# Optimization experiments

Measured on AMD Instinct MI355X. Metric: run time of the kernel, lower is better.

Reference implementation:

```python
import jax, jax.numpy as jnp
import numpy as np

N = 50000      # nodes
E = 800000     # edges (before self loops)
H = 2          # attention heads
CH = 64        # per-head hidden channels
IN = 128       # input features
OUT = 64       # output channels
EPS = 1e-5     # batchnorm eps
SLOPE = 0.2    # LeakyReLU negative slope


def _gat_conv(x, src, dst, W, a_src, a_dst, b, concat):
    # x: [N, Fin]; W: [Fin, H*C]; a_src/a_dst: [H, C]
    n = x.shape[0]
    h = (x @ W).reshape(n, H, -1)                       # [N, H, C]
    al_s = (h * a_src).sum(-1)                          # [N, H]
    al_d = (h * a_dst).sum(-1)                          # [N, H]
    e = al_s[src] + al_d[dst]                           # [E, H]
    e = jnp.where(e > 0, e, SLOPE * e)                  # LeakyReLU
    # softmax over edges grouped by destination node
    m = jax.ops.segment_max(e, dst, num_segments=n)
    ex = jnp.exp(e - m[dst])
    den = jax.ops.segment_sum(ex, dst, num_segments=n)
    alpha = ex / (den[dst] + 1e-16)                     # [E, H]
    out = jax.ops.segment_sum(h[src] * alpha[:, :, None], dst, num_segments=n)
    out = out.reshape(n, -1) if concat else out.mean(axis=1)
    return out + b


def _batchnorm(x, g, be):
    mu = x.mean(axis=0)
    var = x.var(axis=0)  # biased, as torch BN uses in training
    return (x - mu) * jax.lax.rsqrt(var + EPS) * g + be


def setup_inputs() -> dict:
    key = jax.random.key(0)
    ks = jax.random.split(key, 18)
    s = 0.1
    inp = {
        "x": jax.random.normal(ks[0], (N, IN), jnp.float32),
        "edge_index": jax.random.randint(ks[1], (2, E), 0, N, jnp.int64),
        # layer 0: IN -> H*CH (concat)
        "W0": jax.random.normal(ks[2], (IN, H * CH), jnp.float32) * s,
        "a_src0": jax.random.normal(ks[3], (H, CH), jnp.float32) * s,
        "a_dst0": jax.random.normal(ks[4], (H, CH), jnp.float32) * s,
        "b0": jnp.zeros((H * CH,), jnp.float32),
        "g0": jnp.ones((H * CH,), jnp.float32),
        "be0": jnp.zeros((H * CH,), jnp.float32),
        # layer 1: H*CH -> H*CH (concat)
        "W1": jax.random.normal(ks[5], (H * CH, H * CH), jnp.float32) * s,
        "a_src1": jax.random.normal(ks[6], (H, CH), jnp.float32) * s,
        "a_dst1": jax.random.normal(ks[7], (H, CH), jnp.float32) * s,
        "b1": jnp.zeros((H * CH,), jnp.float32),
        "g1": jnp.ones((H * CH,), jnp.float32),
        "be1": jnp.zeros((H * CH,), jnp.float32),
        # layer 2: H*CH -> OUT, concat=False (mean over heads)
        "W2": jax.random.normal(ks[8], (H * CH, H * OUT), jnp.float32) * s,
        "a_src2": jax.random.normal(ks[9], (H, OUT), jnp.float32) * s,
        "a_dst2": jax.random.normal(ks[10], (H, OUT), jnp.float32) * s,
        "b2": jnp.zeros((OUT,), jnp.float32),
    }
    return inp


def reference(x, edge_index, W0, a_src0, a_dst0, b0, g0, be0,
              W1, a_src1, a_dst1, b1, g1, be1,
              W2, a_src2, a_dst2, b2):
    # add self loops (PyG GATConv default)
    loop = jnp.arange(N, dtype=edge_index.dtype)
    src = jnp.concatenate([edge_index[0], loop])
    dst = jnp.concatenate([edge_index[1], loop])

    h = _gat_conv(x, src, dst, W0, a_src0, a_dst0, b0, concat=True)
    h = jax.nn.relu(_batchnorm(h, g0, be0))
    # dropout: eval mode (identity)
    h = _gat_conv(h, src, dst, W1, a_src1, a_dst1, b1, concat=True)
    h = jax.nn.relu(_batchnorm(h, g1, be1))
    out = _gat_conv(h, src, dst, W2, a_src2, a_dst2, b2, concat=False)
    return out
```

## Files before the change

kernel.cpp:

```cpp
#include <hip/hip_runtime.h>


#define N_NODES 50000
#define N_EDGES 800000
#define ET (N_EDGES + N_NODES)
#define FDIM 128
#define SLOPE 0.2f
#define BN_EPS 1e-5f
#define SCAN_NB 196
#define HIST_NB 3321
#define RPK_NB 216
#define LOG2E 1.44269504088896340736f
#define WSTRIDE 18432

typedef __attribute__((ext_vector_type(8))) short bf16x8;
typedef __attribute__((ext_vector_type(4))) float f32x4;
typedef __attribute__((ext_vector_type(8))) unsigned short u16x8;

__device__ __forceinline__ unsigned short f2bf(float f) {
  unsigned u = __float_as_uint(f);
  u = u + 0x7fffu + ((u >> 16) & 1u);
  return (unsigned short)(u >> 16);
}
__device__ __forceinline__ unsigned packbf(float lo, float hi) {
  return ((unsigned)f2bf(hi) << 16) | (unsigned)f2bf(lo);
}
__device__ __forceinline__ float bflo(unsigned p) { return __uint_as_float(p << 16); }
__device__ __forceinline__ float bfhi(unsigned p) { return __uint_as_float(p & 0xffff0000u); }

__global__ __launch_bounds__(256) void build_pre(const int* __restrict__ dst,
                                                 int* __restrict__ counts,
                                                 int* __restrict__ rank,
                                                 const float* __restrict__ W0,
                                                 const float* __restrict__ W1,
                                                 const float* __restrict__ W2,
                                                 const float* __restrict__ as0,
                                                 const float* __restrict__ as1,
                                                 const float* __restrict__ as2,
                                                 const float* __restrict__ ad0,
                                                 const float* __restrict__ ad1,
                                                 const float* __restrict__ ad2,
                                                 unsigned short* __restrict__ Wr) {
  int bid = blockIdx.x;
  if (bid < HIST_NB) {
    int i = bid * 256 + threadIdx.x;
    if (i >= ET) return;
    int d = (i < N_EDGES) ? dst[i] : i - N_EDGES;
    rank[i] = atomicAdd(&counts[d], 1);
    return;
  }
  int i = (bid - HIST_NB) * 256 + threadIdx.x;
  if (i >= 3 * WSTRIDE) return;
  int L = i / WSTRIDE, rem = i % WSTRIDE;
  int t  = rem >> 11;
  int ks = (rem >> 9) & 3;
  int ln = (rem >> 3) & 63;
  int j  = rem & 7;
  int k  = ks * 32 + (ln >> 4) * 8 + j;
  const float* W = (L == 0) ? W0 : ((L == 1) ? W1 : W2);
  float val;
  if (t < 8) {
    int col = t * 16 + (ln & 15);
    val = W[k * 128 + col];
  } else {
    int cl = ln & 15;
    if (cl < 4) {
      int head = cl & 1;
      const float* a = (cl < 2) ? ((L == 0) ? as0 : (L == 1) ? as1 : as2)
                                : ((L == 0) ? ad0 : (L == 1) ? ad1 : ad2);
      float s = 0.f;
      const float* wrow = W + k * 128 + head * 64;
      const float* ah = a + head * 64;
#pragma unroll 8
      for (int c = 0; c < 64; ++c) s = fmaf(wrow[c], ah[c], s);
      val = s * LOG2E;
    } else {
      val = 0.f;
    }
  }
  Wr[i] = f2bf(val);
}


__global__ __launch_bounds__(256) void scan_blk(const int* __restrict__ counts,
                                                int* __restrict__ rowptr,
                                                int* __restrict__ partials) {
  int i = blockIdx.x * 256 + threadIdx.x;
  int lane = threadIdx.x & 63, wv = threadIdx.x >> 6;
  int c = (i < N_NODES) ? counts[i] : 0;
  int v = c;
#pragma unroll
  for (int off = 1; off < 64; off <<= 1) {
    int u = __shfl_up(v, off);
    if (lane >= off) v += u;
  }
  __shared__ int wsum[4];
  if (lane == 63) wsum[wv] = v;
  __syncthreads();
  int add = 0;
  for (int w = 0; w < wv; ++w) add += wsum[w];
  if (i < N_NODES) rowptr[i] = v - c + add;
  if (threadIdx.x == 255) partials[blockIdx.x] = add + v;
}

__global__ __launch_bounds__(256) void scan_fin(int* __restrict__ rowptr,
                                                const int* __restrict__ partials) {
  __shared__ int sh[256];
  int t = threadIdx.x;
  sh[t] = (t < (int)blockIdx.x && t < SCAN_NB) ? partials[t] : 0;
  __syncthreads();
#pragma unroll
  for (int off = 128; off > 0; off >>= 1) {
    if (t < off) sh[t] += sh[t + off];
    __syncthreads();
  }
  int base = sh[0];
  int i = blockIdx.x * 256 + t;
  if (i < N_NODES) rowptr[i] += base;
  if (i == 0) rowptr[N_NODES] = ET;
}

__global__ __launch_bounds__(256) void scatter_pos(const int* __restrict__ src,
                                                   const int* __restrict__ dst,
                                                   const int* __restrict__ rowptr,
                                                   const int* __restrict__ rank,
                                                   int* __restrict__ csr_src) {
  int i = blockIdx.x * 256 + threadIdx.x;
  if (i >= ET) return;
  int d, s;
  if (i < N_EDGES) { d = dst[i]; s = src[i]; } else { d = s = i - N_EDGES; }
  csr_src[rowptr[d] + rank[i]] = s;
}

__global__ __launch_bounds__(128) void bn_fin(float* __restrict__ part,
                                              const float* __restrict__ g,
                                              const float* __restrict__ be,
                                              float* __restrict__ lsbuf) {
  int t = threadIdx.x;
  float s = 0.f, q = 0.f;
#pragma unroll
  for (int k = 0; k < 32; ++k) {
    s += part[k * 256 + t];
    q += part[k * 256 + 128 + t];
    part[k * 256 + t] = 0.f;
    part[k * 256 + 128 + t] = 0.f;
  }
  float mu  = s * (1.f / N_NODES);
  float var = q * (1.f / N_NODES) - mu * mu;
  float sc  = rsqrtf(var + BN_EPS) * g[t];
  lsbuf[t]       = sc;
  lsbuf[128 + t] = be[t] - mu * sc;
}

__global__ __launch_bounds__(256) void gemm_mfma(const void* __restrict__ Xin,
                                                 const unsigned short* __restrict__ WrL,
                                                 const float* __restrict__ lsbuf,
                                                 unsigned short* __restrict__ Hbf,
                                                 float* __restrict__ als,
                                                 float* __restrict__ ald,
                                                 int inBF) {
  __shared__ unsigned short lds[4][16][128];
  __shared__ float ls_scale[128], ls_shift[128];
  int lane = threadIdx.x & 63;
  int wv   = threadIdx.x >> 6;

  if (inBF) {
    int t = threadIdx.x;
    if (t < 128) {
      ls_scale[t] = lsbuf[t];
      ls_shift[t] = lsbuf[128 + t];
    }
    __syncthreads();
  }

  int row0 = blockIdx.x * 64 + wv * 16;
  int gidx = lane & 15;
  int quad = lane >> 4;
  int rA   = row0 + gidx;
  int rAc  = rA < N_NODES ? rA : N_NODES - 1;
  int koff = quad * 8;

  f32x4 acc[9] = {};
#pragma unroll
  for (int ks = 0; ks < 4; ++ks) {
    int cb = ks * 32 + koff;
    float xv[8];
    if (inBF) {
      const uint4* xr = (const uint4*)((const unsigned*)Xin + (size_t)rAc * 64 + (cb >> 1));
      uint4 xa = *xr;
      xv[0] = bflo(xa.x); xv[1] = bfhi(xa.x);
      xv[2] = bflo(xa.y); xv[3] = bfhi(xa.y);
      xv[4] = bflo(xa.z); xv[5] = bfhi(xa.z);
      xv[6] = bflo(xa.w); xv[7] = bfhi(xa.w);
    } else {
      const float4* xr = (const float4*)((const float*)Xin + (size_t)rAc * FDIM + cb);
      float4 xa = xr[0], xb = xr[1];
      xv[0] = xa.x; xv[1] = xa.y; xv[2] = xa.z; xv[3] = xa.w;
      xv[4] = xb.x; xv[5] = xb.y; xv[6] = xb.z; xv[7] = xb.w;
    }
    bf16x8 afrag;
    if (inBF) {
#pragma unroll
      for (int j = 0; j < 8; ++j) {
        int c = cb + j;
        float v = fmaf(xv[j], ls_scale[c], ls_shift[c]);
        v = v > 0.f ? v : 0.f;
        afrag[j] = (short)f2bf(v);
      }
    } else {
#pragma unroll
      for (int j = 0; j < 8; ++j) afrag[j] = (short)f2bf(xv[j]);
    }
#pragma unroll
    for (int t = 0; t < 9; ++t) {
      bf16x8 bfrag = *(const bf16x8*)(WrL + ((size_t)((t * 4 + ks) * 64 + lane)) * 8);
      acc[t] = __builtin_amdgcn_mfma_f32_16x16x32_bf16(afrag, bfrag, acc[t], 0, 0, 0);
    }
  }

  if (gidx < 4) {
    float* dp = (gidx < 2) ? als : ald;
    int hd = gidx & 1;
#pragma unroll
    for (int r = 0; r < 4; ++r) {
      int row = row0 + quad * 4 + r;
      if (row < N_NODES) dp[row * 2 + hd] = acc[8][r];
    }
  }

#pragma unroll
  for (int t = 0; t < 8; ++t)
#pragma unroll
    for (int r = 0; r < 4; ++r)
      lds[wv][quad * 4 + r][t * 16 + gidx] = f2bf(acc[t][r]);
  __syncthreads();
#pragma unroll
  for (int it = 0; it < 4; ++it) {
    int rloc = it * 4 + quad;
    int row = row0 + rloc;
    if (row < N_NODES)
      *(u16x8*)(Hbf + (size_t)row * FDIM + gidx * 8) = *(u16x8*)&lds[wv][rloc][gidx * 8];
  }
}

__global__ __launch_bounds__(256) void fused_agg(const int* __restrict__ rowptr,
                                                 const int* __restrict__ csr_src,
                                                 const unsigned* __restrict__ H2,
                                                 const float* __restrict__ als,
                                                 const float* __restrict__ ald,
                                                 unsigned* __restrict__ Abf,
                                                 float* __restrict__ out,
                                                 const float* __restrict__ b2,
                                                 float* __restrict__ part,
                                                 int mode) {
  int lane = threadIdx.x & 63;
  bool hi = lane >= 32;
  int n = __builtin_amdgcn_readfirstlane((blockIdx.x * 256 + threadIdx.x) >> 6);
  int beg = rowptr[n], end = rowptr[n + 1];
  float2 adv = ((const float2*)ald)[n];
  float advh = hi ? adv.y : adv.x;

  int b0 = end - 8; if (b0 > beg) b0 = beg; if (b0 < 0) b0 = 0;
  int delta = beg - b0;
  int sa[8]; float2 aa[8]; unsigned ha[8];
#pragma unroll
  for (int i = 0; i < 8; ++i) sa[i] = csr_src[b0 + i];
#pragma unroll
  for (int i = 0; i < 8; ++i) {
    aa[i] = ((const float2*)als)[sa[i]];
    ha[i] = H2[(size_t)sa[i] * 64 + lane];
  }

  float l = 0.f, ox = 0.f, oy = 0.f;

#define STEP(i) { \
    float v_ = (hi ? aa[i].y : aa[i].x) + advh; \
    v_ = fmaxf(v_, SLOPE * v_); \
    float e_ = exp2f(v_); \
    l += e_; \
    ox = fmaf(e_, bflo(ha[i]), ox); \
    oy = fmaf(e_, bfhi(ha[i]), oy); }

  int j = beg;
  for (; j + 8 <= end; j += 8) {
    int pp = j + 8; if (pp > end - 8) pp = end - 8;
    int sn[8]; float2 an[8]; unsigned hn[8];
#pragma unroll
    for (int i = 0; i < 8; ++i) sn[i] = csr_src[pp + i];
#pragma unroll
    for (int i = 0; i < 8; ++i) {
      an[i] = ((const float2*)als)[sn[i]];
      hn[i] = H2[(size_t)sn[i] * 64 + lane];
    }
    STEP(0); STEP(1); STEP(2); STEP(3); STEP(4); STEP(5); STEP(6); STEP(7);
    delta = j + 8 - pp;
#pragma unroll
    for (int i = 0; i < 8; ++i) { aa[i] = an[i]; ha[i] = hn[i]; }
  }
  int rem = end - j;
  int hik = delta + rem;
  if (0 >= delta && 0 < hik) STEP(0);
  if (1 >= delta && 1 < hik) STEP(1);
  if (2 >= delta && 2 < hik) STEP(2);
  if (3 >= delta && 3 < hik) STEP(3);
  if (4 >= delta && 4 < hik) STEP(4);
  if (5 >= delta && 5 < hik) STEP(5);
  if (6 >= delta && 6 < hik) STEP(6);
  if (7 >= delta && 7 < hik) STEP(7);
#undef STEP

  float inv = 1.f / (l + 1e-16f);
  ox *= inv; oy *= inv;

  if (mode == 0) {
    Abf[(size_t)n * 64 + lane] = packbf(ox, oy);
    __shared__ float sh[4][4][64];
    int wv = threadIdx.x >> 6;
    sh[wv][0][lane] = ox;
    sh[wv][1][lane] = oy;
    sh[wv][2][lane] = ox * ox;
    sh[wv][3][lane] = oy * oy;
    __syncthreads();
    if (threadIdx.x < 64) {
      int t = threadIdx.x;
      float a0 = 0.f, a1 = 0.f, a2 = 0.f, a3 = 0.f;
#pragma unroll
      for (int w = 0; w < 4; ++w) {
        a0 += sh[w][0][t]; a1 += sh[w][1][t];
        a2 += sh[w][2][t]; a3 += sh[w][3][t];
      }
      float* slot = part + (blockIdx.x & 31) * 256;
      atomicAdd(&slot[2 * t],           a0);
      atomicAdd(&slot[2 * t + 1],       a1);
      atomicAdd(&slot[128 + 2 * t],     a2);
      atomicAdd(&slot[128 + 2 * t + 1], a3);
    }
  } else {
    float px = __shfl_xor(ox, 32);
    float py = __shfl_xor(oy, 32);
    if (lane < 32) {
      int c = lane * 2;
      float2 outv = {0.5f * (ox + px) + b2[c], 0.5f * (oy + py) + b2[c + 1]};
      *(float2*)(out + (size_t)n * 64 + c) = outv;
    }
  }
}

extern "C" void kernel_launch(void* const* d_in, const int* in_sizes, int n_in,
                              void* d_out, int out_size, void* d_ws, size_t ws_size,
                              hipStream_t stream) {
  const float* x  = (const float*)d_in[0];
  const int*   ei = (const int*)d_in[1];
  const int* src = ei;
  const int* dst = ei + N_EDGES;

  const float* W[3]    = {(const float*)d_in[2],  (const float*)d_in[8],  (const float*)d_in[14]};
  const float* asrc[3] = {(const float*)d_in[3],  (const float*)d_in[9],  (const float*)d_in[15]};
  const float* adst[3] = {(const float*)d_in[4],  (const float*)d_in[10], (const float*)d_in[16]};
  const float* g[2]    = {(const float*)d_in[6],  (const float*)d_in[12]};
  const float* be[2]   = {(const float*)d_in[7],  (const float*)d_in[13]};
  const float* b2      = (const float*)d_in[17];

  int*   counts   = (int*)d_ws;
  float* part     = (float*)(counts + 50048);
  int*   rowptr   = (int*)(part + 8192);
  int*   partials = rowptr + 50048;
  int*   rank     = partials + 256;
  int*   csr_src  = rank + 850048;
  float* lsbuf    = (float*)(csr_src + 850048);
  float* als      = lsbuf + 256;
  float* ald      = als + 100096;
  unsigned short* Wr  = (unsigned short*)(ald + 100096);
  unsigned short* Hbf = Wr + 3 * WSTRIDE + 128;
  unsigned* Abf   = (unsigned*)(Hbf + (size_t)N_NODES * FDIM);

  hipMemsetAsync(counts, 0, (50048 + 8192) * sizeof(int), stream);
  build_pre<<<HIST_NB + RPK_NB, 256, 0, stream>>>(
      dst, counts, rank, W[0], W[1], W[2],
      asrc[0], asrc[1], asrc[2], adst[0], adst[1], adst[2], Wr);
  scan_blk<<<SCAN_NB, 256, 0, stream>>>(counts, rowptr, partials);
  scan_fin<<<SCAN_NB, 256, 0, stream>>>(rowptr, partials);
  scatter_pos<<<(ET + 255) / 256, 256, 0, stream>>>(src, dst, rowptr, rank, csr_src);

  const int gemm_grid = (N_NODES + 63) / 64;
  const int agg_grid  = N_NODES * 64 / 256;

  for (int L = 0; L < 3; ++L) {
    const void* fin = (L == 0) ? (const void*)x : (const void*)Abf;
    int inBF = (L > 0);
    gemm_mfma<<<gemm_grid, 256, 0, stream>>>(fin, Wr + (size_t)L * WSTRIDE, lsbuf,
                                             Hbf, als, ald, inBF);
    fused_agg<<<agg_grid, 256, 0, stream>>>(rowptr, csr_src, (const unsigned*)Hbf,
                                            als, ald, Abf, (float*)d_out, b2, part,
                                            (L == 2) ? 2 : 0);
    if (L < 2)
      bn_fin<<<1, 128, 0, stream>>>(part, g[L], be[L], lsbuf);
  }
}
```

Measured before the change: 320.7 us.

## Process two destination nodes per wavefront with 8-byte feature gathers

The aggregation kernel now gives each half-wavefront (32 lanes) its own destination node, with each lane handling four channels loaded as a uint2, so the grid is halved. The edge loop runs for the larger degree of the two nodes, clamps indices, and masks out-of-range edges with a large negative exponent instead of using the tail-offset logic. The BN partial-sum reduction and the head-mean output path are rewritten to match the new lane-to-channel mapping. The aim is to raise gather width and bytes per load for low-degree nodes, at the cost of wasted work when the two paired nodes have very different degrees.

```diff
diff --git a/kernel.cpp b/kernel.cpp
--- a/kernel.cpp
+++ b/kernel.cpp
@@ -254,94 +254,108 @@
                                                  float* __restrict__ part,
                                                  int mode) {
   int lane = threadIdx.x & 63;
-  bool hi = lane >= 32;
-  int n = __builtin_amdgcn_readfirstlane((blockIdx.x * 256 + threadIdx.x) >> 6);
-  int beg = rowptr[n], end = rowptr[n + 1];
-  float2 adv = ((const float2*)ald)[n];
-  float advh = hi ? adv.y : adv.x;
-
-  int b0 = end - 8; if (b0 > beg) b0 = beg; if (b0 < 0) b0 = 0;
-  int delta = beg - b0;
-  int sa[8]; float2 aa[8]; unsigned ha[8];
-#pragma unroll
-  for (int i = 0; i < 8; ++i) sa[i] = csr_src[b0 + i];
+  int sl   = lane & 31;
+  int half = lane >> 5;
+  int head = sl >> 4;
+  int gw = (blockIdx.x * 256 + threadIdx.x) >> 6;
+  int n = gw * 2 + half;
+
+  int beg = rowptr[n];
+  int end = rowptr[n + 1];
+  int deg = end - beg;
+  int degm1 = deg - 1;
+  float advh = ald[(size_t)n * 2 + head];
+
+  int dm = max(deg, __shfl_xor(deg, 32));
+  dm = __builtin_amdgcn_readfirstlane(dm);
+  int nb = (dm + 7) >> 3;
+
+  float av[8]; uint2 ha[8]; int saB[8];
 #pragma unroll
   for (int i = 0; i < 8; ++i) {
-    aa[i] = ((const float2*)als)[sa[i]];
-    ha[i] = H2[(size_t)sa[i] * 64 + lane];
-  }
-
-  float l = 0.f, ox = 0.f, oy = 0.f;
+    int t = i < degm1 ? i : degm1;
+    int s = csr_src[beg + t];
+    av[i] = als[(size_t)s * 2 + head];
+    ha[i] = *(const uint2*)(H2 + (size_t)s * 64 + 2 * sl);
+  }
+#pragma unroll
+  for (int i = 0; i < 8; ++i) {
+    int t = 8 + i; t = t < degm1 ? t : degm1;
+    saB[i] = csr_src[beg + t];
+  }
+
+  float l = 0.f, o0 = 0.f, o1 = 0.f, o2 = 0.f, o3 = 0.f;
+  int rem = deg;
 
 #define STEP(i) { \
-    float v_ = (hi ? aa[i].y : aa[i].x) + advh; \
+    float v_ = av[i] + advh; \
     v_ = fmaxf(v_, SLOPE * v_); \
+    v_ = (i < rem) ? v_ : -1000.f; \
     float e_ = exp2f(v_); \
     l += e_; \
-    ox = fmaf(e_, bflo(ha[i]), ox); \
-    oy = fmaf(e_, bfhi(ha[i]), oy); }
-
-  int j = beg;
-  for (; j + 8 <= end; j += 8) {
-    int pp = j + 8; if (pp > end - 8) pp = end - 8;
-    int sn[8]; float2 an[8]; unsigned hn[8];
-#pragma unroll
-    for (int i = 0; i < 8; ++i) sn[i] = csr_src[pp + i];
+    o0 = fmaf(e_, bflo(ha[i].x), o0); \
+    o1 = fmaf(e_, bfhi(ha[i].x), o1); \
+    o2 = fmaf(e_, bflo(ha[i].y), o2); \
+    o3 = fmaf(e_, bfhi(ha[i].y), o3); }
+
+  for (int b = 0; b + 1 < nb; ++b) {
+    float an[8]; uint2 hn[8];
 #pragma unroll
     for (int i = 0; i < 8; ++i) {
-      an[i] = ((const float2*)als)[sn[i]];
-      hn[i] = H2[(size_t)sn[i] * 64 + lane];
+      an[i] = als[(size_t)saB[i] * 2 + head];
+      hn[i] = *(const uint2*)(H2 + (size_t)saB[i] * 64 + 2 * sl);
+    }
+    int nxt = (b + 2) * 8;
+#pragma unroll
+    for (int i = 0; i < 8; ++i) {
+      int t = nxt + i; t = t < degm1 ? t : degm1;
+      saB[i] = csr_src[beg + t];
     }
     STEP(0); STEP(1); STEP(2); STEP(3); STEP(4); STEP(5); STEP(6); STEP(7);
-    delta = j + 8 - pp;
-#pragma unroll
-    for (int i = 0; i < 8; ++i) { aa[i] = an[i]; ha[i] = hn[i]; }
-  }
-  int rem = end - j;
-  int hik = delta + rem;
-  if (0 >= delta && 0 < hik) STEP(0);
-  if (1 >= delta && 1 < hik) STEP(1);
-  if (2 >= delta && 2 < hik) STEP(2);
-  if (3 >= delta && 3 < hik) STEP(3);
-  if (4 >= delta && 4 < hik) STEP(4);
-  if (5 >= delta && 5 < hik) STEP(5);
-  if (6 >= delta && 6 < hik) STEP(6);
-  if (7 >= delta && 7 < hik) STEP(7);
+    rem -= 8;
+#pragma unroll
+    for (int i = 0; i < 8; ++i) { av[i] = an[i]; ha[i] = hn[i]; }
+  }
+  STEP(0); STEP(1); STEP(2); STEP(3); STEP(4); STEP(5); STEP(6); STEP(7);
 #undef STEP
 
   float inv = 1.f / (l + 1e-16f);
-  ox *= inv; oy *= inv;
+  o0 *= inv; o1 *= inv; o2 *= inv; o3 *= inv;
 
   if (mode == 0) {
-    Abf[(size_t)n * 64 + lane] = packbf(ox, oy);
-    __shared__ float sh[4][4][64];
+    uint2 pk = { packbf(o0, o1), packbf(o2, o3) };
+    *(uint2*)(Abf + (size_t)n * 64 + 2 * sl) = pk;
+    __shared__ float sh[4][2][32][4];
     int wv = threadIdx.x >> 6;
-    sh[wv][0][lane] = ox;
-    sh[wv][1][lane] = oy;
-    sh[wv][2][lane] = ox * ox;
-    sh[wv][3][lane] = oy * oy;
+    float4 quad = { o0, o1, o2, o3 };
+    *(float4*)&sh[wv][half][sl][0] = quad;
     __syncthreads();
-    if (threadIdx.x < 64) {
-      int t = threadIdx.x;
-      float a0 = 0.f, a1 = 0.f, a2 = 0.f, a3 = 0.f;
-#pragma unroll
-      for (int w = 0; w < 4; ++w) {
-        a0 += sh[w][0][t]; a1 += sh[w][1][t];
-        a2 += sh[w][2][t]; a3 += sh[w][3][t];
-      }
+    if (threadIdx.x < 128) {
+      int c = threadIdx.x;
+      int q = c >> 2, r = c & 3;
+      float a = 0.f, asq = 0.f;
+#pragma unroll
+      for (int w = 0; w < 4; ++w)
+#pragma unroll
+        for (int hh = 0; hh < 2; ++hh) {
+          float v = sh[w][hh][q][r];
+          a += v; asq += v * v;
+        }
       float* slot = part + (blockIdx.x & 31) * 256;
-      atomicAdd(&slot[2 * t],           a0);
-      atomicAdd(&slot[2 * t + 1],       a1);
-      atomicAdd(&slot[128 + 2 * t],     a2);
-      atomicAdd(&slot[128 + 2 * t + 1], a3);
+      atomicAdd(&slot[c], a);
+      atomicAdd(&slot[128 + c], asq);
     }
   } else {
-    float px = __shfl_xor(ox, 32);
-    float py = __shfl_xor(oy, 32);
-    if (lane < 32) {
-      int c = lane * 2;
-      float2 outv = {0.5f * (ox + px) + b2[c], 0.5f * (oy + py) + b2[c + 1]};
-      *(float2*)(out + (size_t)n * 64 + c) = outv;
+    float p0 = __shfl_xor(o0, 16);
+    float p1 = __shfl_xor(o1, 16);
+    float p2 = __shfl_xor(o2, 16);
+    float p3 = __shfl_xor(o3, 16);
+    if (head == 0) {
+      int c = sl * 4;
+      float4 bv = *(const float4*)(b2 + c);
+      float4 ov = { 0.5f * (o0 + p0) + bv.x, 0.5f * (o1 + p1) + bv.y,
+                    0.5f * (o2 + p2) + bv.z, 0.5f * (o3 + p3) + bv.w };
+      *(float4*)(out + (size_t)n * 64 + c) = ov;
     }
   }
 }
@@ -383,7 +397,7 @@
   scatter_pos<<<(ET + 255) / 256, 256, 0, stream>>>(src, dst, rowptr, rank, csr_src);
 
   const int gemm_grid = (N_NODES + 63) / 64;
-  const int agg_grid  = N_NODES * 64 / 256;
+  const int agg_grid  = N_NODES / 8;
 
   for (int L = 0; L < 3; ++L) {
     const void* fin = (L == 0) ? (const void*)x : (const void*)Abf;
```

Result: slower. 330.1 us (+2.9%).

## Move batchnorm statistics out of aggregation into separate reduction kernel; simplify tail loop

Applied to the files above, without the earlier changes.

Removes the per-block shared-memory reduction, the __syncthreads and the global atomicAdds for batchnorm sums from the aggregation kernel. A new 32-block bn_stats kernel instead re-reads the bf16 aggregated features and writes per-block partial sums without atomics. The edge loop is also restructured to process full groups of 8 plus a masked remainder, using clamped indices rather than an overlapping window, so fewer edges are loaded redundantly. The cost is an extra kernel launch and an extra pass over the features per layer, run on only 32 blocks. The statistics are now computed from bf16-rounded values rather than fp32.

```diff
diff --git a/kernel.cpp b/kernel.cpp
--- a/kernel.cpp
+++ b/kernel.cpp
@@ -12,6 +12,8 @@
 #define RPK_NB 216
 #define LOG2E 1.44269504088896340736f
 #define WSTRIDE 18432
+#define BNS_NB 32
+#define BNS_STRIDE 1563
 
 typedef __attribute__((ext_vector_type(8))) short bf16x8;
 typedef __attribute__((ext_vector_type(4))) float f32x4;
@@ -132,6 +134,40 @@
   csr_src[rowptr[d] + rank[i]] = s;
 }
 
+__global__ __launch_bounds__(256) void bn_stats(const unsigned* __restrict__ Abf,
+                                                float* __restrict__ part) {
+  int tid = threadIdx.x;
+  int j = tid & 63;
+  int rg = tid >> 6;
+  int rs = blockIdx.x * BNS_STRIDE;
+  int re = rs + BNS_STRIDE;
+  if (re > N_NODES) re = N_NODES;
+  float sx = 0.f, sy = 0.f, qx = 0.f, qy = 0.f;
+  for (int r = rs + rg; r < re; r += 4) {
+    unsigned u = Abf[(size_t)r * 64 + j];
+    float x = bflo(u), y = bfhi(u);
+    sx += x; sy += y;
+    qx = fmaf(x, x, qx); qy = fmaf(y, y, qy);
+  }
+  __shared__ float red[4][4][64];
+  red[rg][0][j] = sx; red[rg][1][j] = sy;
+  red[rg][2][j] = qx; red[rg][3][j] = qy;
+  __syncthreads();
+  if (tid < 64) {
+    float a0 = 0.f, a1 = 0.f, a2 = 0.f, a3 = 0.f;
+#pragma unroll
+    for (int w = 0; w < 4; ++w) {
+      a0 += red[w][0][tid]; a1 += red[w][1][tid];
+      a2 += red[w][2][tid]; a3 += red[w][3][tid];
+    }
+    float* slot = part + blockIdx.x * 256;
+    slot[2 * tid]           = a0;
+    slot[2 * tid + 1]       = a1;
+    slot[128 + 2 * tid]     = a2;
+    slot[128 + 2 * tid + 1] = a3;
+  }
+}
+
 __global__ __launch_bounds__(128) void bn_fin(float* __restrict__ part,
                                               const float* __restrict__ g,
                                               const float* __restrict__ be,
@@ -251,20 +287,25 @@
                                                  unsigned* __restrict__ Abf,
                                                  float* __restrict__ out,
                                                  const float* __restrict__ b2,
-                                                 float* __restrict__ part,
                                                  int mode) {
   int lane = threadIdx.x & 63;
   bool hi = lane >= 32;
   int n = __builtin_amdgcn_readfirstlane((blockIdx.x * 256 + threadIdx.x) >> 6);
   int beg = rowptr[n], end = rowptr[n + 1];
+  int deg = end - beg;
+  int last = end - 1;
   float2 adv = ((const float2*)ald)[n];
   float advh = hi ? adv.y : adv.x;
 
-  int b0 = end - 8; if (b0 > beg) b0 = beg; if (b0 < 0) b0 = 0;
-  int delta = beg - b0;
+  int nfull = deg >> 3;
+  int rem = deg & 7;
+
   int sa[8]; float2 aa[8]; unsigned ha[8];
 #pragma unroll
-  for (int i = 0; i < 8; ++i) sa[i] = csr_src[b0 + i];
+  for (int i = 0; i < 8; ++i) {
+    int idx = beg + i; idx = idx > last ? last : idx;
+    sa[i] = csr_src[idx];
+  }
 #pragma unroll
   for (int i = 0; i < 8; ++i) {
     aa[i] = ((const float2*)als)[sa[i]];
@@ -273,68 +314,82 @@
 
   float l = 0.f, ox = 0.f, oy = 0.f;
 
-#define STEP(i) { \
+#define STEPU(i) { \
     float v_ = (hi ? aa[i].y : aa[i].x) + advh; \
     v_ = fmaxf(v_, SLOPE * v_); \
     float e_ = exp2f(v_); \
     l += e_; \
     ox = fmaf(e_, bflo(ha[i]), ox); \
     oy = fmaf(e_, bfhi(ha[i]), oy); }
-
-  int j = beg;
-  for (; j + 8 <= end; j += 8) {
-    int pp = j + 8; if (pp > end - 8) pp = end - 8;
+#define STEPM(i) { if (i < rem) STEPU(i) }
+
+  for (int b = 1; b < nfull; ++b) {
+    int base = beg + b * 8;
     int sn[8]; float2 an[8]; unsigned hn[8];
 #pragma unroll
-    for (int i = 0; i < 8; ++i) sn[i] = csr_src[pp + i];
+    for (int i = 0; i < 8; ++i) sn[i] = csr_src[base + i];
 #pragma unroll
     for (int i = 0; i < 8; ++i) {
       an[i] = ((const float2*)als)[sn[i]];
       hn[i] = H2[(size_t)sn[i] * 64 + lane];
     }
-    STEP(0); STEP(1); STEP(2); STEP(3); STEP(4); STEP(5); STEP(6); STEP(7);
-    delta = j + 8 - pp;
+    STEPU(0); STEPU(1); STEPU(2); STEPU(3);
+    STEPU(4); STEPU(5); STEPU(6); STEPU(7);
 #pragma unroll
     for (int i = 0; i < 8; ++i) { aa[i] = an[i]; ha[i] = hn[i]; }
   }
-  int rem = end - j;
-  int hik = delta + rem;
-  if (0 >= delta && 0 < hik) STEP(0);
-  if (1 >= delta && 1 < hik) STEP(1);
-  if (2 >= delta && 2 < hik) STEP(2);
-  if (3 >= delta && 3 < hik) STEP(3);
-  if (4 >= delta && 4 < hik) STEP(4);
-  if (5 >= delta && 5 < hik) STEP(5);
-  if (6 >= delta && 6 < hik) STEP(6);
-  if (7 >= delta && 7 < hik) STEP(7);
-#undef STEP
+
+  if (nfull) {
+    int base = beg + nfull * 8;
+    int sn[8]; float2 an[8]; unsigned hn[8];
+    if (rem > 4) {
+#pragma unroll
+      for (int i = 0; i < 8; ++i) {
+        int idx = base + i; idx = idx > last ? last : idx;
+        sn[i] = csr_src[idx];
+      }
+#pragma unroll
+      for (int i = 0; i < 8; ++i) {
+        an[i] = ((const float2*)als)[sn[i]];
+        hn[i] = H2[(size_t)sn[i] * 64 + lane];
+      }
+    } else if (rem) {
+#pragma unroll
+      for (int i = 0; i < 4; ++i) {
+        int idx = base + i; idx = idx > last ? last : idx;
+        sn[i] = csr_src[idx];
+      }
+#pragma unroll
+      for (int i = 0; i < 4; ++i) {
+        an[i] = ((const float2*)als)[sn[i]];
+        hn[i] = H2[(size_t)sn[i] * 64 + lane];
+      }
+    }
+    STEPU(0); STEPU(1); STEPU(2); STEPU(3);
+    STEPU(4); STEPU(5); STEPU(6); STEPU(7);
+    if (rem > 4) {
+#pragma unroll
+      for (int i = 0; i < 8; ++i) { aa[i] = an[i]; ha[i] = hn[i]; }
+    } else if (rem) {
+#pragma unroll
+      for (int i = 0; i < 4; ++i) { aa[i] = an[i]; ha[i] = hn[i]; }
+    }
+  }
+
+  if (rem > 4) {
+    STEPM(0); STEPM(1); STEPM(2); STEPM(3);
+    STEPM(4); STEPM(5); STEPM(6); STEPM(7);
+  } else if (rem) {
+    STEPM(0); STEPM(1); STEPM(2); STEPM(3);
+  }
+#undef STEPU
+#undef STEPM
 
   float inv = 1.f / (l + 1e-16f);
   ox *= inv; oy *= inv;
 
   if (mode == 0) {
     Abf[(size_t)n * 64 + lane] = packbf(ox, oy);
-    __shared__ float sh[4][4][64];
-    int wv = threadIdx.x >> 6;
-    sh[wv][0][lane] = ox;
-    sh[wv][1][lane] = oy;
-    sh[wv][2][lane] = ox * ox;
-    sh[wv][3][lane] = oy * oy;
-    __syncthreads();
-    if (threadIdx.x < 64) {
-      int t = threadIdx.x;
-      float a0 = 0.f, a1 = 0.f, a2 = 0.f, a3 = 0.f;
-#pragma unroll
-      for (int w = 0; w < 4; ++w) {
-        a0 += sh[w][0][t]; a1 += sh[w][1][t];
-        a2 += sh[w][2][t]; a3 += sh[w][3][t];
-      }
-      float* slot = part + (blockIdx.x & 31) * 256;
-      atomicAdd(&slot[2 * t],           a0);
-      atomicAdd(&slot[2 * t + 1],       a1);
-      atomicAdd(&slot[128 + 2 * t],     a2);
-      atomicAdd(&slot[128 + 2 * t + 1], a3);
-    }
   } else {
     float px = __shfl_xor(ox, 32);
     float py = __shfl_xor(oy, 32);
@@ -391,9 +446,11 @@
     gemm_mfma<<<gemm_grid, 256, 0, stream>>>(fin, Wr + (size_t)L * WSTRIDE, lsbuf,
                                              Hbf, als, ald, inBF);
     fused_agg<<<agg_grid, 256, 0, stream>>>(rowptr, csr_src, (const unsigned*)Hbf,
-                                            als, ald, Abf, (float*)d_out, b2, part,
+                                            als, ald, Abf, (float*)d_out, b2,
                                             (L == 2) ? 2 : 0);
-    if (L < 2)
+    if (L < 2) {
+      bn_stats<<<BNS_NB, 256, 0, stream>>>(Abf, part);
       bn_fin<<<1, 128, 0, stream>>>(part, g[L], be[L], lsbuf);
-  }
-}
+    }
+  }
+}
```

Result: slower. 522.2 us (+62.9%).
